# Performance work log

Measured on AMD Instinct MI355X. Metric: run time of the kernel, lower is better.

## Reference

```python
import jax, jax.numpy as jnp
import numpy as np

N_NODES = 50000
N_EDGES = 800000
D_IN = 128
D_OUT = 128


def setup_inputs() -> dict:
    key = jax.random.key(0)
    k_feat, k_src, k_dst, k_ws, k_bs, k_wn = jax.random.split(key, 6)
    feat = jax.random.normal(k_feat, (N_NODES, D_IN), dtype=jnp.float32)
    src = jax.random.randint(k_src, (N_EDGES,), 0, N_NODES, dtype=jnp.int64)
    dst = jax.random.randint(k_dst, (N_EDGES,), 0, N_NODES, dtype=jnp.int64)
    # fc_self: Linear(D_IN, D_OUT, bias=True); fc_neigh: Linear(D_IN, D_OUT, bias=False)
    W_self = jax.random.normal(k_ws, (D_OUT, D_IN), dtype=jnp.float32) * (1.0 / np.sqrt(D_IN))
    b_self = jax.random.normal(k_bs, (D_OUT,), dtype=jnp.float32) * 0.01
    # xavier_uniform with relu gain
    gain = float(np.sqrt(2.0))
    bound = gain * float(np.sqrt(6.0 / (D_IN + D_OUT)))
    W_neigh = jax.random.uniform(k_wn, (D_OUT, D_IN), dtype=jnp.float32, minval=-bound, maxval=bound)
    bias = jnp.zeros((D_OUT,), dtype=jnp.float32)
    return {"feat": feat, "src": src, "dst": dst, "W_self": W_self,
            "b_self": b_self, "W_neigh": W_neigh, "bias": bias}


def reference(feat, src, dst, W_self, b_self, W_neigh, bias):
    # copy_u('h','m') + fn.mean('m','neigh'): gather src feats, mean-reduce by dst.
    # lin_before_mp is False (in_feats == out_feats), so aggregate raw feats first.
    n = feat.shape[0]
    msgs = feat[src]                                             # [E, D_IN]
    neigh_sum = jax.ops.segment_sum(msgs, dst, num_segments=n)   # [N, D_IN]
    deg = jax.ops.segment_sum(jnp.ones(src.shape, feat.dtype), dst, num_segments=n)
    # DGL mean yields 0 for zero-in-degree nodes
    h_neigh = jnp.where(deg[:, None] > 0, neigh_sum / jnp.maximum(deg, 1.0)[:, None], 0.0)
    h_neigh = h_neigh @ W_neigh.T                                # fc_neigh (no bias)
    h_self = feat @ W_self.T + b_self                            # fc_self
    return h_self + h_neigh + bias
```

## Files before the change

### kernel.cpp

```cpp
#include <hip/hip_runtime.h>
#include <hip/hip_fp8.h>

#define N_NODES 50000
#define N_EDGES 800000
#define D 128
#define NBUK 782
#define CAPB 1344
#define SRTN (CAPB + 64*3)
#define PCHUNK 2048
#define SCAT_BLOCKS 391
#define FEAT_BLOCKS 3125
#define W_BLOCKS 32
#define CURS 16

typedef __bf16 bf16x8 __attribute__((ext_vector_type(8)));
typedef __bf16 bf16x4 __attribute__((ext_vector_type(4)));
typedef float  f32x4  __attribute__((ext_vector_type(4)));
typedef float  f32x2  __attribute__((ext_vector_type(2)));

#if defined(__has_builtin)
#if __has_builtin(__builtin_amdgcn_cvt_pk_f32_fp8) && __has_builtin(__builtin_amdgcn_cvt_pk_fp8_f32)
#define HW_FP8 1
#endif
#endif

#define OFF_GCURSOR 0ull
#define OFF_PACKED  50176ull
#define OFF_FEAT8   4254208ull
#define OFF_WC16    10654336ull
#define OFF_BIASC   10719872ull
#define OFF_FEAT16  10720384ull

__device__ __forceinline__ float fp8tof_sw(unsigned char b) {
    __hip_fp8_e4m3 t; t.__x = b;
    return (float)t;
}

__global__ __launch_bounds__(256)
void prep_kernel(const int* __restrict__ src, const int* __restrict__ dst,
                 int* __restrict__ gcursor, int* __restrict__ packed,
                 const float* __restrict__ feat, unsigned char* __restrict__ feat8,
                 __bf16* __restrict__ feat16,
                 const float* __restrict__ Ws, const float* __restrict__ Wn,
                 const float* __restrict__ b_self, const float* __restrict__ bias,
                 __bf16* __restrict__ Wc16, float* __restrict__ biasc, int n) {
    const int tid = threadIdx.x;
    const int bid = blockIdx.x;
    if (bid < SCAT_BLOCKS) {
        __shared__ int lh[NBUK];
        __shared__ int lbase[NBUK];
        const int e0 = bid * PCHUNK;
        int d[8], s[8];
        for (int i = tid; i < NBUK; i += 256) lh[i] = 0;
        __syncthreads();
        #pragma unroll
        for (int j = 0; j < 8; ++j) {
            int e = e0 + j * 256 + tid;
            bool ok = e < n;
            d[j] = ok ? dst[e] : -1;
            s[j] = ok ? src[e] : 0;
            if (ok) atomicAdd(&lh[d[j] >> 6], 1);
        }
        __syncthreads();
        for (int i = tid; i < NBUK; i += 256) {
            int c = lh[i];
            lbase[i] = c ? atomicAdd(&gcursor[i * CURS], c) : 0;
            lh[i] = 0;
        }
        __syncthreads();
        #pragma unroll
        for (int j = 0; j < 8; ++j) {
            if (d[j] >= 0) {
                int bk = d[j] >> 6;
                int r = atomicAdd(&lh[bk], 1);
                int pos = lbase[bk] + r;
                if (pos < CAPB)
                    packed[(size_t)bk * CAPB + pos] = ((d[j] & 63) << 16) | s[j];
            }
        }
    } else if (bid < SCAT_BLOCKS + FEAT_BLOCKS) {
        size_t i = ((size_t)(bid - SCAT_BLOCKS) * 256 + tid) * 8;
        float4 f0 = *(const float4*)(feat + i);
        float4 f1 = *(const float4*)(feat + i + 4);
        bf16x8 t16;
        t16[0]=(__bf16)f0.x; t16[1]=(__bf16)f0.y; t16[2]=(__bf16)f0.z; t16[3]=(__bf16)f0.w;
        t16[4]=(__bf16)f1.x; t16[5]=(__bf16)f1.y; t16[6]=(__bf16)f1.z; t16[7]=(__bf16)f1.w;
        *(bf16x8*)(feat16 + i) = t16;
#ifdef HW_FP8
        int q0 = __builtin_amdgcn_cvt_pk_fp8_f32(f0.x, f0.y, 0, false);
        q0     = __builtin_amdgcn_cvt_pk_fp8_f32(f0.z, f0.w, q0, true);
        int q1 = __builtin_amdgcn_cvt_pk_fp8_f32(f1.x, f1.y, 0, false);
        q1     = __builtin_amdgcn_cvt_pk_fp8_f32(f1.z, f1.w, q1, true);
        uint2 qq; qq.x = (unsigned)q0; qq.y = (unsigned)q1;
        *(uint2*)(feat8 + i) = qq;
#else
        float fv[8] = {f0.x, f0.y, f0.z, f0.w, f1.x, f1.y, f1.z, f1.w};
        union { unsigned char b[8]; unsigned long long u; } q;
        #pragma unroll
        for (int j = 0; j < 8; ++j) { __hip_fp8_e4m3 e(fv[j]); q.b[j] = e.__x; }
        *(unsigned long long*)(feat8 + i) = q.u;
#endif
    } else if (bid < SCAT_BLOCKS + FEAT_BLOCKS + W_BLOCKS) {
        int idx = (bid - SCAT_BLOCKS - FEAT_BLOCKS) * 256 + tid;
        int col = idx >> 6;
        int kq  = (idx & 63) * 4;
        const float* srcp = (kq < D) ? (Ws + (size_t)col * D + kq)
                                     : (Wn + (size_t)col * D + (kq - D));
        float4 f = *(const float4*)srcp;
        bf16x4 t;
        t[0]=(__bf16)f.x; t[1]=(__bf16)f.y; t[2]=(__bf16)f.z; t[3]=(__bf16)f.w;
        *(bf16x4*)(Wc16 + (size_t)col * 256 + kq) = t;
    } else {
        if (tid < D) biasc[tid] = b_self[tid] + bias[tid];
        else if (tid < D + 32)
            ((unsigned*)(feat8 + (size_t)N_NODES * D))[tid - 128] = 0u;
    }
}

__global__ __launch_bounds__(512, 8)
void fused_kernel(const __bf16* __restrict__ feat16,
                  const unsigned char* __restrict__ feat8,
                  const int* __restrict__ gcursor,
                  const int* __restrict__ packed,
                  const __bf16* __restrict__ Wc16,
                  const float* __restrict__ biasc,
                  float* __restrict__ out) {
    __shared__ __align__(16) char smem[64 * 264 * 2];
    __shared__ unsigned short srt[SRTN];
    __shared__ int cnt[64];
    __shared__ int loff[64];
    __shared__ int degs[64];
    __bf16 (*At)[264] = (__bf16 (*)[264])smem;
    int* pk = (int*)smem;
    const int tid = threadIdx.x;
    const int b = blockIdx.x;
    const int node0 = b * 64;
    const int ecnt = min(gcursor[b * CURS], CAPB);

    const int srow = tid >> 3;
    const int scol = (tid & 7) * 16;
    const int snn = node0 + srow;
    bf16x8 st0 = {}, st1 = {};
    if (snn < N_NODES) {
        const __bf16* sp = feat16 + (size_t)snn * D + scol;
        st0 = *(const bf16x8*)sp;
        st1 = *(const bf16x8*)(sp + 8);
    }

    if (tid < 64) cnt[tid] = 0;
    for (int i = tid; i < ecnt; i += 512) pk[i] = packed[(size_t)b * CAPB + i];
    __syncthreads();

    for (int i = tid; i < ecnt; i += 512) atomicAdd(&cnt[pk[i] >> 16], 1);
    __syncthreads();
    if (tid < 64) {
        int c = cnt[tid];
        int cp = (c + 3) & ~3;
        int v = cp;
        #pragma unroll
        for (int o = 1; o < 64; o <<= 1) {
            int u = __shfl_up(v, o);
            if (tid >= o) v += u;
        }
        loff[tid] = v - cp;
        degs[tid] = c;
        cnt[tid] = 0;
    }
    __syncthreads();
    for (int i = tid; i < ecnt; i += 512) {
        int p = pk[i];
        int l = p >> 16;
        int r = atomicAdd(&cnt[l], 1);
        srt[loff[l] + r] = (unsigned short)p;
    }
    if (tid < 64) {
        int c = degs[tid];
        int cp = (c + 3) & ~3;
        int base0 = loff[tid];
        for (int j = c; j < cp; ++j) srt[base0 + j] = (unsigned short)N_NODES;
    }
    __syncthreads();

    *(bf16x8*)&At[srow][scol] = st0;
    *(bf16x8*)&At[srow][scol + 8] = st1;

    {
        const int hw = tid >> 5;
        const int lane = tid & 31;
        const unsigned int* g8 = (const unsigned int*)feat8;
        #pragma unroll
        for (int t = 0; t < 4; ++t) {
            int i = hw + t * 16;
            int dg = degs[i];
            int dgp = (dg + 3) & ~3;
            const int base0 = loff[i];
            float a0 = 0.f, a1 = 0.f, a2 = 0.f, a3 = 0.f;
            for (int j = 0; j < dgp; j += 4) {
                unsigned int w[4];
                #pragma unroll
                for (int q = 0; q < 4; ++q) {
                    int s = srt[base0 + j + q];
                    w[q] = g8[(size_t)s * 32 + lane];
                }
                #pragma unroll
                for (int q = 0; q < 4; ++q) {
#ifdef HW_FP8
                    f32x2 lo = __builtin_amdgcn_cvt_pk_f32_fp8((int)w[q], false);
                    f32x2 hi = __builtin_amdgcn_cvt_pk_f32_fp8((int)w[q], true);
                    a0 += lo[0]; a1 += lo[1]; a2 += hi[0]; a3 += hi[1];
#else
                    a0 += fp8tof_sw(w[q] & 0xFF);
                    a1 += fp8tof_sw((w[q] >> 8) & 0xFF);
                    a2 += fp8tof_sw((w[q] >> 16) & 0xFF);
                    a3 += fp8tof_sw(w[q] >> 24);
#endif
                }
            }
            float sc = dg > 0 ? 1.0f / (float)dg : 0.f;
            bf16x4 hv;
            hv[0] = (__bf16)(a0 * sc); hv[1] = (__bf16)(a1 * sc);
            hv[2] = (__bf16)(a2 * sc); hv[3] = (__bf16)(a3 * sc);
            *(bf16x4*)&At[i][128 + lane * 4] = hv;
        }
    }
    __syncthreads();

    const int wv = tid >> 6;
    const int lane = tid & 63;
    const int m = lane & 15;
    const int quad = lane >> 4;
    const int r0 = (wv & 1) * 32;
    const int c0 = (wv >> 1) * 32;

    f32x4 acc[2][2] = {};
    #pragma unroll
    for (int k0 = 0; k0 < 256; k0 += 32) {
        const int kk = k0 + quad * 8;
        bf16x8 a0 = *(const bf16x8*)&At[r0 + m][kk];
        bf16x8 a1 = *(const bf16x8*)&At[r0 + 16 + m][kk];
        #pragma unroll
        for (int ct = 0; ct < 2; ++ct) {
            int col = c0 + ct * 16 + m;
            bf16x8 bb = *(const bf16x8*)(Wc16 + (size_t)col * 256 + kk);
            acc[0][ct] = __builtin_amdgcn_mfma_f32_16x16x32_bf16(a0, bb, acc[0][ct], 0, 0, 0);
            acc[1][ct] = __builtin_amdgcn_mfma_f32_16x16x32_bf16(a1, bb, acc[1][ct], 0, 0, 0);
        }
    }
    __syncthreads();

    float* Ct = (float*)smem;
    #pragma unroll
    for (int rt = 0; rt < 2; ++rt) {
        #pragma unroll
        for (int ct = 0; ct < 2; ++ct) {
            int ccol = c0 + ct * 16 + m;
            int crow = r0 + rt * 16 + quad * 4;
            #pragma unroll
            for (int r = 0; r < 4; ++r)
                Ct[(crow + r) * 132 + ccol] = acc[rt][ct][r];
        }
    }
    __syncthreads();
    for (int idx = tid; idx < 64 * 32; idx += 512) {
        int row = idx >> 5;
        int c4 = (idx & 31) * 4;
        int nn = node0 + row;
        if (nn < N_NODES) {
            float4 v = *(float4*)&Ct[row * 132 + c4];
            float4 bb = *(const float4*)(biasc + c4);
            v.x += bb.x; v.y += bb.y; v.z += bb.z; v.w += bb.w;
            *(float4*)&out[(size_t)nn * D + c4] = v;
        }
    }
}

extern "C" void kernel_launch(void* const* d_in, const int* in_sizes, int n_in,
                              void* d_out, int out_size, void* d_ws, size_t ws_size,
                              hipStream_t stream) {
    const float* feat    = (const float*)d_in[0];
    const int*   src     = (const int*)d_in[1];
    const int*   dst     = (const int*)d_in[2];
    const float* W_self  = (const float*)d_in[3];
    const float* b_self  = (const float*)d_in[4];
    const float* W_neigh = (const float*)d_in[5];
    const float* bias    = (const float*)d_in[6];
    float* out = (float*)d_out;
    char*  ws  = (char*)d_ws;

    int* gcursor = (int*)(ws + OFF_GCURSOR);
    int* packed  = (int*)(ws + OFF_PACKED);
    unsigned char* feat8 = (unsigned char*)(ws + OFF_FEAT8);
    __bf16* Wc16   = (__bf16*)(ws + OFF_WC16);
    float*  biasc  = (float*)(ws + OFF_BIASC);
    __bf16* feat16 = (__bf16*)(ws + OFF_FEAT16);
    const int n_edges = in_sizes[1];

    hipMemsetAsync(gcursor, 0, 50176, stream);
    prep_kernel<<<dim3(SCAT_BLOCKS + FEAT_BLOCKS + W_BLOCKS + 1), 256, 0, stream>>>(
        src, dst, gcursor, packed, feat, feat8, feat16, W_self, W_neigh,
        b_self, bias, Wc16, biasc, n_edges);
    fused_kernel<<<dim3(NBUK), 512, 0, stream>>>(
        feat16, feat8, gcursor, packed, Wc16, biasc, out);
}
```

Measured before the change: 147.4 us.

## Fuse prep and aggregation kernels into one launch with a grid barrier

Merges the prep kernel (edge bucketing, fp8/bf16 feature conversion, weight packing) into the main fused kernel, using a global atomic spin barrier so that all 782 blocks finish bucketing before aggregation starts. Each block now converts its own 64 self-feature rows straight from fp32 into registers, which removes the bf16 feature buffer's write and re-read. This saves one kernel launch and the gap between kernels. In exchange, all 782 blocks must be co-resident for the barrier to be safe, and the bucketing phase runs at only 1024 edges per block. Wc16 and biasc are written by blocks 0 to 16 and read after the barrier, but only the atomic acquire/release orders those writes.

```diff
diff --git a/kernel.cpp b/kernel.cpp
--- a/kernel.cpp
+++ b/kernel.cpp
@@ -7,10 +7,7 @@
 #define NBUK 782
 #define CAPB 1344
 #define SRTN (CAPB + 64*3)
-#define PCHUNK 2048
-#define SCAT_BLOCKS 391
-#define FEAT_BLOCKS 3125
-#define W_BLOCKS 32
+#define EPB 1024
 #define CURS 16
 
 typedef __bf16 bf16x8 __attribute__((ext_vector_type(8)));
@@ -25,83 +22,72 @@
 #endif
 
 #define OFF_GCURSOR 0ull
-#define OFF_PACKED  50176ull
-#define OFF_FEAT8   4254208ull
-#define OFF_WC16    10654336ull
-#define OFF_BIASC   10719872ull
-#define OFF_FEAT16  10720384ull
+#define OFF_BAR     50176ull
+#define OFF_PACKED  51200ull
+#define OFF_FEAT8   4255232ull
+#define OFF_WC16    10655360ull
+#define OFF_BIASC   10720896ull
 
 __device__ __forceinline__ float fp8tof_sw(unsigned char b) {
     __hip_fp8_e4m3 t; t.__x = b;
     return (float)t;
 }
 
-__global__ __launch_bounds__(256)
-void prep_kernel(const int* __restrict__ src, const int* __restrict__ dst,
-                 int* __restrict__ gcursor, int* __restrict__ packed,
+__global__ __launch_bounds__(512, 8)
+void mega_kernel(const int* __restrict__ src, const int* __restrict__ dst,
+                 int* __restrict__ gcursor, int* __restrict__ bar,
+                 int* __restrict__ packed,
                  const float* __restrict__ feat, unsigned char* __restrict__ feat8,
-                 __bf16* __restrict__ feat16,
                  const float* __restrict__ Ws, const float* __restrict__ Wn,
                  const float* __restrict__ b_self, const float* __restrict__ bias,
-                 __bf16* __restrict__ Wc16, float* __restrict__ biasc, int n) {
+                 __bf16* __restrict__ Wc16, float* __restrict__ biasc,
+                 float* __restrict__ out, int n) {
+    __shared__ __align__(16) char smem[64 * 264 * 2];
+    __shared__ unsigned short srt[SRTN];
+    __shared__ int cnt[64];
+    __shared__ int loff[64];
+    __shared__ int degs[64];
     const int tid = threadIdx.x;
-    const int bid = blockIdx.x;
-    if (bid < SCAT_BLOCKS) {
-        __shared__ int lh[NBUK];
-        __shared__ int lbase[NBUK];
-        const int e0 = bid * PCHUNK;
-        int d[8], s[8];
-        for (int i = tid; i < NBUK; i += 256) lh[i] = 0;
-        __syncthreads();
-        #pragma unroll
-        for (int j = 0; j < 8; ++j) {
-            int e = e0 + j * 256 + tid;
-            bool ok = e < n;
-            d[j] = ok ? dst[e] : -1;
-            s[j] = ok ? src[e] : 0;
-            if (ok) atomicAdd(&lh[d[j] >> 6], 1);
-        }
-        __syncthreads();
-        for (int i = tid; i < NBUK; i += 256) {
-            int c = lh[i];
-            lbase[i] = c ? atomicAdd(&gcursor[i * CURS], c) : 0;
-            lh[i] = 0;
-        }
-        __syncthreads();
-        #pragma unroll
-        for (int j = 0; j < 8; ++j) {
-            if (d[j] >= 0) {
-                int bk = d[j] >> 6;
-                int r = atomicAdd(&lh[bk], 1);
-                int pos = lbase[bk] + r;
-                if (pos < CAPB)
-                    packed[(size_t)bk * CAPB + pos] = ((d[j] & 63) << 16) | s[j];
-            }
-        }
-    } else if (bid < SCAT_BLOCKS + FEAT_BLOCKS) {
-        size_t i = ((size_t)(bid - SCAT_BLOCKS) * 256 + tid) * 8;
-        float4 f0 = *(const float4*)(feat + i);
-        float4 f1 = *(const float4*)(feat + i + 4);
-        bf16x8 t16;
-        t16[0]=(__bf16)f0.x; t16[1]=(__bf16)f0.y; t16[2]=(__bf16)f0.z; t16[3]=(__bf16)f0.w;
-        t16[4]=(__bf16)f1.x; t16[5]=(__bf16)f1.y; t16[6]=(__bf16)f1.z; t16[7]=(__bf16)f1.w;
-        *(bf16x8*)(feat16 + i) = t16;
+    const int b = blockIdx.x;
+    const int node0 = b * 64;
+
+    const int srow = tid >> 3;
+    const int scol = (tid & 7) * 16;
+    const int snn = node0 + srow;
+    bf16x8 st0 = {}, st1 = {};
+    if (snn < N_NODES) {
+        const float* fp = feat + (size_t)snn * D + scol;
+        float4 f0 = *(const float4*)(fp);
+        float4 f1 = *(const float4*)(fp + 4);
+        float4 f2 = *(const float4*)(fp + 8);
+        float4 f3 = *(const float4*)(fp + 12);
+        st0[0]=(__bf16)f0.x; st0[1]=(__bf16)f0.y; st0[2]=(__bf16)f0.z; st0[3]=(__bf16)f0.w;
+        st0[4]=(__bf16)f1.x; st0[5]=(__bf16)f1.y; st0[6]=(__bf16)f1.z; st0[7]=(__bf16)f1.w;
+        st1[0]=(__bf16)f2.x; st1[1]=(__bf16)f2.y; st1[2]=(__bf16)f2.z; st1[3]=(__bf16)f2.w;
+        st1[4]=(__bf16)f3.x; st1[5]=(__bf16)f3.y; st1[6]=(__bf16)f3.z; st1[7]=(__bf16)f3.w;
 #ifdef HW_FP8
         int q0 = __builtin_amdgcn_cvt_pk_fp8_f32(f0.x, f0.y, 0, false);
         q0     = __builtin_amdgcn_cvt_pk_fp8_f32(f0.z, f0.w, q0, true);
         int q1 = __builtin_amdgcn_cvt_pk_fp8_f32(f1.x, f1.y, 0, false);
         q1     = __builtin_amdgcn_cvt_pk_fp8_f32(f1.z, f1.w, q1, true);
-        uint2 qq; qq.x = (unsigned)q0; qq.y = (unsigned)q1;
-        *(uint2*)(feat8 + i) = qq;
+        int q2 = __builtin_amdgcn_cvt_pk_fp8_f32(f2.x, f2.y, 0, false);
+        q2     = __builtin_amdgcn_cvt_pk_fp8_f32(f2.z, f2.w, q2, true);
+        int q3 = __builtin_amdgcn_cvt_pk_fp8_f32(f3.x, f3.y, 0, false);
+        q3     = __builtin_amdgcn_cvt_pk_fp8_f32(f3.z, f3.w, q3, true);
+        uint4 qq; qq.x=(unsigned)q0; qq.y=(unsigned)q1; qq.z=(unsigned)q2; qq.w=(unsigned)q3;
+        *(uint4*)(feat8 + (size_t)snn * D + scol) = qq;
 #else
-        float fv[8] = {f0.x, f0.y, f0.z, f0.w, f1.x, f1.y, f1.z, f1.w};
-        union { unsigned char b[8]; unsigned long long u; } q;
-        #pragma unroll
-        for (int j = 0; j < 8; ++j) { __hip_fp8_e4m3 e(fv[j]); q.b[j] = e.__x; }
-        *(unsigned long long*)(feat8 + i) = q.u;
+        float fv[16] = {f0.x,f0.y,f0.z,f0.w, f1.x,f1.y,f1.z,f1.w,
+                        f2.x,f2.y,f2.z,f2.w, f3.x,f3.y,f3.z,f3.w};
+        union { unsigned char c[16]; uint4 u; } q;
+        #pragma unroll
+        for (int j = 0; j < 16; ++j) { __hip_fp8_e4m3 e(fv[j]); q.c[j] = e.__x; }
+        *(uint4*)(feat8 + (size_t)snn * D + scol) = q.u;
 #endif
-    } else if (bid < SCAT_BLOCKS + FEAT_BLOCKS + W_BLOCKS) {
-        int idx = (bid - SCAT_BLOCKS - FEAT_BLOCKS) * 256 + tid;
+    }
+
+    if (b < 16) {
+        int idx = b * 512 + tid;
         int col = idx >> 6;
         int kq  = (idx & 63) * 4;
         const float* srcp = (kq < D) ? (Ws + (size_t)col * D + kq)
@@ -110,42 +96,56 @@
         bf16x4 t;
         t[0]=(__bf16)f.x; t[1]=(__bf16)f.y; t[2]=(__bf16)f.z; t[3]=(__bf16)f.w;
         *(bf16x4*)(Wc16 + (size_t)col * 256 + kq) = t;
-    } else {
+    } else if (b == 16) {
         if (tid < D) biasc[tid] = b_self[tid] + bias[tid];
         else if (tid < D + 32)
             ((unsigned*)(feat8 + (size_t)N_NODES * D))[tid - 128] = 0u;
     }
-}
-
-__global__ __launch_bounds__(512, 8)
-void fused_kernel(const __bf16* __restrict__ feat16,
-                  const unsigned char* __restrict__ feat8,
-                  const int* __restrict__ gcursor,
-                  const int* __restrict__ packed,
-                  const __bf16* __restrict__ Wc16,
-                  const float* __restrict__ biasc,
-                  float* __restrict__ out) {
-    __shared__ __align__(16) char smem[64 * 264 * 2];
-    __shared__ unsigned short srt[SRTN];
-    __shared__ int cnt[64];
-    __shared__ int loff[64];
-    __shared__ int degs[64];
+
+    {
+        int* lh = (int*)smem;
+        int* lbase = lh + NBUK;
+        for (int i = tid; i < NBUK; i += 512) lh[i] = 0;
+        __syncthreads();
+        const int e0 = b * EPB;
+        int ea = e0 + tid, eb = e0 + 512 + tid;
+        int d0 = -1, s0 = 0, d1 = -1, s1 = 0;
+        if (ea < n) { d0 = dst[ea]; s0 = src[ea]; }
+        if (eb < n) { d1 = dst[eb]; s1 = src[eb]; }
+        if (d0 >= 0) atomicAdd(&lh[d0 >> 6], 1);
+        if (d1 >= 0) atomicAdd(&lh[d1 >> 6], 1);
+        __syncthreads();
+        for (int i = tid; i < NBUK; i += 512) {
+            int c = lh[i];
+            lbase[i] = c ? atomicAdd(&gcursor[i * CURS], c) : 0;
+            lh[i] = 0;
+        }
+        __syncthreads();
+        if (d0 >= 0) {
+            int bk = d0 >> 6;
+            int r = atomicAdd(&lh[bk], 1);
+            int pos = lbase[bk] + r;
+            if (pos < CAPB) packed[(size_t)bk * CAPB + pos] = ((d0 & 63) << 16) | s0;
+        }
+        if (d1 >= 0) {
+            int bk = d1 >> 6;
+            int r = atomicAdd(&lh[bk], 1);
+            int pos = lbase[bk] + r;
+            if (pos < CAPB) packed[(size_t)bk * CAPB + pos] = ((d1 & 63) << 16) | s1;
+        }
+    }
+    __syncthreads();
+
+    if (tid == 0) {
+        __hip_atomic_fetch_add(bar, 1, __ATOMIC_ACQ_REL, __HIP_MEMORY_SCOPE_AGENT);
+        while (__hip_atomic_load(bar, __ATOMIC_ACQUIRE, __HIP_MEMORY_SCOPE_AGENT) < NBUK)
+            __builtin_amdgcn_s_sleep(8);
+    }
+    __syncthreads();
+
     __bf16 (*At)[264] = (__bf16 (*)[264])smem;
     int* pk = (int*)smem;
-    const int tid = threadIdx.x;
-    const int b = blockIdx.x;
-    const int node0 = b * 64;
     const int ecnt = min(gcursor[b * CURS], CAPB);
-
-    const int srow = tid >> 3;
-    const int scol = (tid & 7) * 16;
-    const int snn = node0 + srow;
-    bf16x8 st0 = {}, st1 = {};
-    if (snn < N_NODES) {
-        const __bf16* sp = feat16 + (size_t)snn * D + scol;
-        st0 = *(const bf16x8*)sp;
-        st1 = *(const bf16x8*)(sp + 8);
-    }
 
     if (tid < 64) cnt[tid] = 0;
     for (int i = tid; i < ecnt; i += 512) pk[i] = packed[(size_t)b * CAPB + i];
@@ -288,17 +288,15 @@
     char*  ws  = (char*)d_ws;
 
     int* gcursor = (int*)(ws + OFF_GCURSOR);
+    int* bar     = (int*)(ws + OFF_BAR);
     int* packed  = (int*)(ws + OFF_PACKED);
     unsigned char* feat8 = (unsigned char*)(ws + OFF_FEAT8);
-    __bf16* Wc16   = (__bf16*)(ws + OFF_WC16);
-    float*  biasc  = (float*)(ws + OFF_BIASC);
-    __bf16* feat16 = (__bf16*)(ws + OFF_FEAT16);
+    __bf16* Wc16  = (__bf16*)(ws + OFF_WC16);
+    float*  biasc = (float*)(ws + OFF_BIASC);
     const int n_edges = in_sizes[1];
 
-    hipMemsetAsync(gcursor, 0, 50176, stream);
-    prep_kernel<<<dim3(SCAT_BLOCKS + FEAT_BLOCKS + W_BLOCKS + 1), 256, 0, stream>>>(
-        src, dst, gcursor, packed, feat, feat8, feat16, W_self, W_neigh,
-        b_self, bias, Wc16, biasc, n_edges);
-    fused_kernel<<<dim3(NBUK), 512, 0, stream>>>(
-        feat16, feat8, gcursor, packed, Wc16, biasc, out);
+    hipMemsetAsync(ws, 0, 51200, stream);
+    mega_kernel<<<dim3(NBUK), 512, 0, stream>>>(
+        src, dst, gcursor, bar, packed, feat, feat8,
+        W_self, W_neigh, b_self, bias, Wc16, biasc, out, n_edges);
 }
```

Result: slower. 265.4 us (+80.0%).
